# Kernel tuning notes

Hardware: AMD Instinct MI355X
Metric: run time of the kernel (lower is better)

Reference implementation:

```python
import jax, jax.numpy as jnp
import numpy as np

N_NODES = 100000


def setup_inputs() -> dict:
    key = jax.random.key(0)
    ks = jax.random.split(key, 7)
    n, d, c, e = N_NODES, 256, 128, 3200000
    features = jax.random.normal(ks[0], (n, d), dtype=jnp.float32)
    adj_row = jax.random.randint(ks[1], (e,), 0, n, dtype=jnp.int32)
    adj_col = jax.random.randint(ks[2], (e,), 0, n, dtype=jnp.int32)
    adj_vals = jax.random.uniform(ks[3], (e,), dtype=jnp.float32)
    kernel = jax.random.normal(ks[4], (d, c), dtype=jnp.float32) * (1.0 / np.sqrt(d))
    bias = jax.random.normal(ks[5], (c,), dtype=jnp.float32) * 0.01
    skip_weight = jax.random.normal(ks[6], (c,), dtype=jnp.float32)
    return {"features": features, "adj_row": adj_row, "adj_col": adj_col,
            "adj_vals": adj_vals, "kernel": kernel, "bias": bias,
            "skip_weight": skip_weight}


def reference(features, adj_row, adj_col, adj_vals, kernel, bias, skip_weight):
    # h = X @ W  : [n, c]
    h = features @ kernel
    # SpMM: out[r] += A[r, c] * h[c] over edges (COO)
    msgs = adj_vals[:, None] * h[adj_col]            # [e, c]
    agg = jax.ops.segment_sum(msgs, adj_row, num_segments=N_NODES)  # [n, c]
    out = h * skip_weight + agg                      # skip-connection scale + aggregation
    out = out + bias
    return jax.nn.selu(out)
```

## Files before the change

### kernel.cpp

```cpp
#include <hip/hip_runtime.h>
#include <math.h>

#define N_NODES 100000
#define D 256
#define C 128
#define N_EDGES 3200000

#define BROWS 64
#define NBUCKET ((N_NODES + BROWS - 1) / BROWS)
#define CAP 2432
#define EPB 8192
#define PBLOCKS ((N_EDGES + EPB - 1) / EPB)

#define GROWS 128
#define NGB ((N_NODES + GROWS - 1) / GROWS)
#define KH 128
#define XPAD 136

typedef __attribute__((ext_vector_type(8))) short bf16x8;
typedef __attribute__((ext_vector_type(4))) float f32x4;

__device__ __forceinline__ unsigned short f2bf(float f) {
  const unsigned int u = __float_as_uint(f);
  return (unsigned short)((u + 0x7fffu + ((u >> 16) & 1u)) >> 16);
}
__device__ __forceinline__ unsigned int pack_bf(float lo, float hi) {
  return (unsigned int)f2bf(lo) | ((unsigned int)f2bf(hi) << 16);
}
__device__ __forceinline__ float bflo(unsigned int u) {
  return __uint_as_float(u << 16);
}
__device__ __forceinline__ float bfhi(unsigned int u) {
  return __uint_as_float(u & 0xffff0000u);
}
__device__ __forceinline__ float selu1(float x) {
  const float scale = 1.0507009873554804934193349852946f;
  const float alpha = 1.6732632423543772848170429916717f;
  return x > 0.f ? scale * x : scale * alpha * (__expf(x) - 1.f);
}
__device__ __forceinline__ unsigned int pack_rec(int col, float val) {
  return ((unsigned int)col << 15) | ((unsigned int)f2bf(val) & 0x7fffu);
}
__device__ __forceinline__ float rec_val(unsigned int r) {
  return __uint_as_float((r & 0x7fffu) << 16);
}
__device__ __forceinline__ bf16x8 packA_nt(const float* p) {
  const f32x4 a0 = __builtin_nontemporal_load(reinterpret_cast<const f32x4*>(p));
  const f32x4 a1 =
      __builtin_nontemporal_load(reinterpret_cast<const f32x4*>(p) + 1);
  union {
    unsigned int u[4];
    bf16x8 v;
  } af;
  af.u[0] = pack_bf(a0[0], a0[1]);
  af.u[1] = pack_bf(a0[2], a0[3]);
  af.u[2] = pack_bf(a1[0], a1[1]);
  af.u[3] = pack_bf(a1[2], a1[3]);
  return af.v;
}

__global__ __launch_bounds__(256) void prep(const float* __restrict__ W,
                                            unsigned short* __restrict__ WT) {
  const int t = blockIdx.x * blockDim.x + threadIdx.x;
  const int n = t >> 8;
  const int k = t & 255;
  WT[t] = f2bf(W[k * C + n]);
}

__global__ __launch_bounds__(512) void gemm_partition(
    const float* __restrict__ X, const unsigned short* __restrict__ WT,
    unsigned short* __restrict__ h2, const int* __restrict__ row,
    const int* __restrict__ col, const float* __restrict__ vals,
    unsigned int* __restrict__ meta, uint2* __restrict__ recs) {
  __shared__ alignas(16) char smem[GROWS * XPAD * 2];
  const int bid = blockIdx.x;
  const int tid = threadIdx.x;
  const int rem = bid % 3;

  if (rem != 2) {
    unsigned short(*xs)[XPAD] = reinterpret_cast<unsigned short(*)[XPAD]>(smem);
    const int gid = (bid / 3) * 2 + rem;
    const int rows0 = gid * GROWS;
    const int lane = tid & 63;
    const int w = tid >> 6;
    const int r = lane & 15;
    const int kg = lane >> 4;

    f32x4 acc[8];
#pragma unroll
    for (int f = 0; f < 8; ++f) acc[f] = (f32x4){0.f, 0.f, 0.f, 0.f};

#pragma unroll
    for (int h = 0; h < 2; ++h) {
#pragma unroll
      for (int i = 0; i < 8; ++i) {
        const int lrow = w * 16 + i * 2 + (lane >> 5);
        const int grow = rows0 + lrow;
        const int kc = (lane & 31) * 4;
        f32x4 x = (f32x4){0.f, 0.f, 0.f, 0.f};
        if (grow < N_NODES)
          x = *reinterpret_cast<const f32x4*>(X + (size_t)grow * D + h * KH +
                                              kc);
        const unsigned int p0 = pack_bf(x[0], x[1]);
        const unsigned int p1 = pack_bf(x[2], x[3]);
        *reinterpret_cast<uint2*>(&xs[lrow][kc]) = make_uint2(p0, p1);
      }
      __syncthreads();
#pragma unroll
      for (int ks = 0; ks < 4; ++ks) {
        const bf16x8 a =
            *reinterpret_cast<const bf16x8*>(&xs[w * 16 + r][ks * 32 + kg * 8]);
#pragma unroll
        for (int f = 0; f < 8; ++f) {
          const bf16x8 bf = *reinterpret_cast<const bf16x8*>(
              WT + (size_t)(f * 16 + r) * D + h * KH + ks * 32 + kg * 8);
          acc[f] =
              __builtin_amdgcn_mfma_f32_16x16x32_bf16(a, bf, acc[f], 0, 0, 0);
        }
      }
      __syncthreads();
    }
#pragma unroll
    for (int f = 0; f < 8; ++f)
#pragma unroll
      for (int j = 0; j < 4; ++j) {
        const int grow = rows0 + w * 16 + kg * 4 + j;
        if (grow < N_NODES) h2[(size_t)grow * C + f * 16 + r] = f2bf(acc[f][j]);
      }
  } else {
    int* hist = reinterpret_cast<int*>(smem);
    int* scanA = reinterpret_cast<int*>(smem + 8192);
    int* scanB = reinterpret_cast<int*>(smem + 16384);
    const int pb = bid / 3;
    const int e0 = pb * EPB;
    for (int i = tid; i < NBUCKET; i += 512) hist[i] = 0;
    __syncthreads();

    unsigned int stash[16];
#pragma unroll
    for (int k = 0; k < 16; ++k) {
      const int e = e0 + k * 512 + tid;
      unsigned int s = 0xFFFFFFFFu;
      if (e < N_EDGES) {
        const int r = __builtin_nontemporal_load(row + e);
        const int off = atomicAdd(&hist[r >> 6], 1);
        s = (unsigned int)r | ((unsigned int)off << 17);
      }
      stash[k] = s;
    }
    __syncthreads();

    for (int i = tid; i < 2048; i += 512) scanA[i] = (i < NBUCKET) ? hist[i] : 0;
    __syncthreads();
    int* src = scanA;
    int* dst = scanB;
    for (int off = 1; off < 2048; off <<= 1) {
      for (int i = tid; i < 2048; i += 512)
        dst[i] = src[i] + ((i >= off) ? src[i - off] : 0);
      __syncthreads();
      int* tp = src;
      src = dst;
      dst = tp;
    }
    for (int b = tid; b < NBUCKET; b += 512) {
      const int sb = src[b] - hist[b];
      dst[b] = sb;
      meta[(size_t)pb * NBUCKET + b] =
          ((unsigned int)sb << 16) | (unsigned int)hist[b];
    }
    __syncthreads();

#pragma unroll
    for (int k = 0; k < 16; ++k) {
      const unsigned int s = stash[k];
      if (s == 0xFFFFFFFFu) continue;
      const int r = (int)(s & 0x1FFFFu);
      const int off = (int)(s >> 17);
      const int e = e0 + k * 512 + tid;
      const int c = __builtin_nontemporal_load(col + e);
      const float v = __builtin_nontemporal_load(vals + e);
      const int b = r >> 6;
      recs[(size_t)pb * EPB + dst[b] + off] =
          make_uint2(pack_rec(c, v), r & (BROWS - 1));
    }
  }
}

__global__ __launch_bounds__(256) void sort_gather_selu(
    const unsigned int* __restrict__ meta, const uint2* __restrict__ recs,
    const unsigned int* __restrict__ h2u, const float* __restrict__ skip,
    const float* __restrict__ bias, float* __restrict__ out) {
  __shared__ unsigned int sorted[CAP];
  __shared__ int hist[BROWS];
  __shared__ int start[BROWS];
  __shared__ int segA[512];
  __shared__ int segB[512];
  __shared__ unsigned int segglob[512];
  const int tid = threadIdx.x;
  const int b = blockIdx.x;

  for (int s = tid; s < 512; s += 256) {
    int cnt = 0;
    unsigned int gg = 0;
    if (s < PBLOCKS) {
      const unsigned int m = meta[(size_t)s * NBUCKET + b];
      cnt = (int)(m & 0xFFFFu);
      gg = (unsigned int)s * EPB + (m >> 16);
    }
    segA[s] = cnt;
    segglob[s] = gg;
  }
  if (tid < BROWS) hist[tid] = 0;
  __syncthreads();
  int* s1 = segA;
  int* s2 = segB;
  for (int off = 1; off < 512; off <<= 1) {
    for (int i = tid; i < 512; i += 256)
      s2[i] = s1[i] + ((i >= off) ? s1[i - off] : 0);
    __syncthreads();
    int* tp = s1;
    s1 = s2;
    s2 = tp;
  }
  const int fill0 = s1[PBLOCKS - 1];
  const int fill = fill0 < CAP ? fill0 : CAP;

  uint2 stash[10];
  int nst = 0;
  for (int i = tid; i < fill; i += 256) {
    int lo = 0, hi = PBLOCKS - 1;
    while (lo < hi) {
      const int mid = (lo + hi) >> 1;
      if (s1[mid] > i) hi = mid;
      else lo = mid + 1;
    }
    const int idx = i - (lo ? s1[lo - 1] : 0);
    const unsigned long long rc = __builtin_nontemporal_load(
        reinterpret_cast<const unsigned long long*>(recs) + segglob[lo] + idx);
    const unsigned int cv = (unsigned int)rc;
    const unsigned int lr = (unsigned int)(rc >> 32);
    const int off = atomicAdd(&hist[lr], 1);
    stash[nst] = make_uint2(cv, lr | ((unsigned int)off << 6));
    ++nst;
  }
  __syncthreads();

  if (tid < BROWS) start[tid] = hist[tid];
  __syncthreads();
  for (int off = 1; off < BROWS; off <<= 1) {
    int t = 0;
    if (tid < BROWS && tid >= off) t = start[tid - off];
    __syncthreads();
    if (tid < BROWS) start[tid] += t;
    __syncthreads();
  }

  for (int k = 0; k < nst; ++k) {
    const int lr = (int)(stash[k].y & 63u);
    const int off = (int)(stash[k].y >> 6);
    const int pos = start[lr] - hist[lr] + off;
    if (pos < CAP) sorted[pos] = stash[k].x;
  }
  __syncthreads();

  const int lane = tid & 63;
  const int wv = tid >> 6;
  for (int lr = wv; lr < BROWS; lr += 4) {
    const int grow = b * BROWS + lr;
    if (grow >= N_NODES) break;
    int j = start[lr] - hist[lr];
    int je = start[lr];
    if (je > CAP) je = CAP;
    if (j > je) j = je;
    float ax = 0.f, ay = 0.f;
    for (; j + 7 < je; j += 8) {
      unsigned int cc[8], uu[8];
#pragma unroll
      for (int q = 0; q < 8; ++q) cc[q] = sorted[j + q];
#pragma unroll
      for (int q = 0; q < 8; ++q) uu[q] = h2u[(size_t)(cc[q] >> 15) * 64 + lane];
#pragma unroll
      for (int q = 0; q < 8; ++q) {
        ax = fmaf(rec_val(cc[q]), bflo(uu[q]), ax);
        ay = fmaf(rec_val(cc[q]), bfhi(uu[q]), ay);
      }
    }
    for (; j + 3 < je; j += 4) {
      unsigned int cc[4], uu[4];
#pragma unroll
      for (int q = 0; q < 4; ++q) cc[q] = sorted[j + q];
#pragma unroll
      for (int q = 0; q < 4; ++q) uu[q] = h2u[(size_t)(cc[q] >> 15) * 64 + lane];
#pragma unroll
      for (int q = 0; q < 4; ++q) {
        ax = fmaf(rec_val(cc[q]), bflo(uu[q]), ax);
        ay = fmaf(rec_val(cc[q]), bfhi(uu[q]), ay);
      }
    }
    for (; j < je; ++j) {
      const unsigned int cc = sorted[j];
      const unsigned int u = h2u[(size_t)(cc >> 15) * 64 + lane];
      ax = fmaf(rec_val(cc), bflo(u), ax);
      ay = fmaf(rec_val(cc), bfhi(u), ay);
    }
    const unsigned int hr = h2u[(size_t)grow * 64 + lane];
    const float2 sk = *reinterpret_cast<const float2*>(skip + lane * 2);
    const float2 bi = *reinterpret_cast<const float2*>(bias + lane * 2);
    const float ox = selu1(fmaf(bflo(hr), sk.x, ax) + bi.x);
    const float oy = selu1(fmaf(bfhi(hr), sk.y, ay) + bi.y);
    *reinterpret_cast<float2*>(out + (size_t)grow * C + lane * 2) =
        make_float2(ox, oy);
  }
}

extern "C" void kernel_launch(void* const* d_in, const int* in_sizes, int n_in,
                              void* d_out, int out_size, void* d_ws,
                              size_t ws_size, hipStream_t stream) {
  const float* features = (const float*)d_in[0];
  const int* adj_row = (const int*)d_in[1];
  const int* adj_col = (const int*)d_in[2];
  const float* adj_vals = (const float*)d_in[3];
  const float* W = (const float*)d_in[4];
  const float* bias = (const float*)d_in[5];
  const float* skip = (const float*)d_in[6];
  float* out = (float*)d_out;

  char* ws = (char*)d_ws;
  const size_t SZ_H2 = (size_t)N_NODES * C * 2;
  const size_t OFF_RECS = (SZ_H2 + 255) & ~(size_t)255;
  const size_t SZ_RECS = (size_t)PBLOCKS * EPB * 8;
  const size_t OFF_META = OFF_RECS + SZ_RECS;
  const size_t SZ_META = (size_t)PBLOCKS * NBUCKET * 4;
  const size_t OFF_WT = (OFF_META + SZ_META + 255) & ~(size_t)255;
  const size_t NEEDED = OFF_WT + (size_t)D * C * 2;

  if (ws_size < NEEDED) return;

  unsigned short* h2 = (unsigned short*)ws;
  uint2* recs = (uint2*)(ws + OFF_RECS);
  unsigned int* meta = (unsigned int*)(ws + OFF_META);
  unsigned short* WT = (unsigned short*)(ws + OFF_WT);

  prep<<<(D * C) / 256, 256, 0, stream>>>(W, WT);

  gemm_partition<<<3 * PBLOCKS, 512, 0, stream>>>(
      features, WT, h2, adj_row, adj_col, adj_vals, meta, recs);

  sort_gather_selu<<<NBUCKET, 256, 0, stream>>>(
      meta, recs, (const unsigned int*)h2, skip, bias, out);
}
```

Baseline: 271.6 us.

## Co-schedule GEMM with bucket sort and split partition into its own kernel

Edge partitioning moves into a standalone kernel. The per-bucket sort now runs alongside the GEMM in one heterogeneous launch, writing sorted records and row pointers to global memory. A lean gather+SELU kernel then reads the presorted data. This aims to hide the sort under the GEMM and shorten the gather kernel, at the cost of an extra launch and an extra global round trip for the sorted records.

```diff
diff --git a/kernel.cpp b/kernel.cpp
--- a/kernel.cpp
+++ b/kernel.cpp
@@ -43,20 +43,6 @@
 }
 __device__ __forceinline__ float rec_val(unsigned int r) {
   return __uint_as_float((r & 0x7fffu) << 16);
-}
-__device__ __forceinline__ bf16x8 packA_nt(const float* p) {
-  const f32x4 a0 = __builtin_nontemporal_load(reinterpret_cast<const f32x4*>(p));
-  const f32x4 a1 =
-      __builtin_nontemporal_load(reinterpret_cast<const f32x4*>(p) + 1);
-  union {
-    unsigned int u[4];
-    bf16x8 v;
-  } af;
-  af.u[0] = pack_bf(a0[0], a0[1]);
-  af.u[1] = pack_bf(a0[2], a0[3]);
-  af.u[2] = pack_bf(a1[0], a1[1]);
-  af.u[3] = pack_bf(a1[2], a1[3]);
-  return af.v;
 }
 
 __global__ __launch_bounds__(256) void prep(const float* __restrict__ W,
@@ -67,19 +53,81 @@
   WT[t] = f2bf(W[k * C + n]);
 }
 
-__global__ __launch_bounds__(512) void gemm_partition(
+__global__ __launch_bounds__(512) void partition_kernel(
+    const int* __restrict__ row, const int* __restrict__ col,
+    const float* __restrict__ vals, unsigned int* __restrict__ meta,
+    uint2* __restrict__ recs) {
+  __shared__ int hist[2048];
+  __shared__ int scanA[2048];
+  __shared__ int scanB[2048];
+  const int pb = blockIdx.x;
+  const int tid = threadIdx.x;
+  const int e0 = pb * EPB;
+  for (int i = tid; i < NBUCKET; i += 512) hist[i] = 0;
+  __syncthreads();
+
+  unsigned int stash[16];
+#pragma unroll
+  for (int k = 0; k < 16; ++k) {
+    const int e = e0 + k * 512 + tid;
+    unsigned int s = 0xFFFFFFFFu;
+    if (e < N_EDGES) {
+      const int r = __builtin_nontemporal_load(row + e);
+      const int off = atomicAdd(&hist[r >> 6], 1);
+      s = (unsigned int)r | ((unsigned int)off << 17);
+    }
+    stash[k] = s;
+  }
+  __syncthreads();
+
+  for (int i = tid; i < 2048; i += 512) scanA[i] = (i < NBUCKET) ? hist[i] : 0;
+  __syncthreads();
+  int* src = scanA;
+  int* dst = scanB;
+  for (int off = 1; off < 2048; off <<= 1) {
+    for (int i = tid; i < 2048; i += 512)
+      dst[i] = src[i] + ((i >= off) ? src[i - off] : 0);
+    __syncthreads();
+    int* tp = src;
+    src = dst;
+    dst = tp;
+  }
+  for (int b = tid; b < NBUCKET; b += 512) {
+    const int sb = src[b] - hist[b];
+    dst[b] = sb;
+    meta[(size_t)pb * NBUCKET + b] =
+        ((unsigned int)sb << 16) | (unsigned int)hist[b];
+  }
+  __syncthreads();
+
+#pragma unroll
+  for (int k = 0; k < 16; ++k) {
+    const unsigned int s = stash[k];
+    if (s == 0xFFFFFFFFu) continue;
+    const int r = (int)(s & 0x1FFFFu);
+    const int off = (int)(s >> 17);
+    const int e = e0 + k * 512 + tid;
+    const int c = __builtin_nontemporal_load(col + e);
+    const float v = __builtin_nontemporal_load(vals + e);
+    const int b = r >> 6;
+    recs[(size_t)pb * EPB + dst[b] + off] =
+        make_uint2(pack_rec(c, v), r & (BROWS - 1));
+  }
+}
+
+__global__ __launch_bounds__(512) void gemm_sort(
     const float* __restrict__ X, const unsigned short* __restrict__ WT,
-    unsigned short* __restrict__ h2, const int* __restrict__ row,
-    const int* __restrict__ col, const float* __restrict__ vals,
-    unsigned int* __restrict__ meta, uint2* __restrict__ recs) {
+    unsigned short* __restrict__ h2, const unsigned int* __restrict__ meta,
+    const uint2* __restrict__ recs, unsigned int* __restrict__ sorted_g,
+    int* __restrict__ rowptr_g) {
   __shared__ alignas(16) char smem[GROWS * XPAD * 2];
   const int bid = blockIdx.x;
   const int tid = threadIdx.x;
   const int rem = bid % 3;
 
-  if (rem != 2) {
+  if (rem == 0) {
     unsigned short(*xs)[XPAD] = reinterpret_cast<unsigned short(*)[XPAD]>(smem);
-    const int gid = (bid / 3) * 2 + rem;
+    const int gid = bid / 3;
     const int rows0 = gid * GROWS;
     const int lane = tid & 63;
     const int w = tid >> 6;
@@ -128,155 +176,108 @@
         if (grow < N_NODES) h2[(size_t)grow * C + f * 16 + r] = f2bf(acc[f][j]);
       }
   } else {
-    int* hist = reinterpret_cast<int*>(smem);
-    int* scanA = reinterpret_cast<int*>(smem + 8192);
-    int* scanB = reinterpret_cast<int*>(smem + 16384);
-    const int pb = bid / 3;
-    const int e0 = pb * EPB;
-    for (int i = tid; i < NBUCKET; i += 512) hist[i] = 0;
-    __syncthreads();
-
-    unsigned int stash[16];
-#pragma unroll
-    for (int k = 0; k < 16; ++k) {
-      const int e = e0 + k * 512 + tid;
-      unsigned int s = 0xFFFFFFFFu;
-      if (e < N_EDGES) {
-        const int r = __builtin_nontemporal_load(row + e);
-        const int off = atomicAdd(&hist[r >> 6], 1);
-        s = (unsigned int)r | ((unsigned int)off << 17);
-      }
-      stash[k] = s;
-    }
-    __syncthreads();
-
-    for (int i = tid; i < 2048; i += 512) scanA[i] = (i < NBUCKET) ? hist[i] : 0;
-    __syncthreads();
-    int* src = scanA;
-    int* dst = scanB;
-    for (int off = 1; off < 2048; off <<= 1) {
-      for (int i = tid; i < 2048; i += 512)
-        dst[i] = src[i] + ((i >= off) ? src[i - off] : 0);
-      __syncthreads();
-      int* tp = src;
-      src = dst;
-      dst = tp;
-    }
-    for (int b = tid; b < NBUCKET; b += 512) {
-      const int sb = src[b] - hist[b];
-      dst[b] = sb;
-      meta[(size_t)pb * NBUCKET + b] =
-          ((unsigned int)sb << 16) | (unsigned int)hist[b];
-    }
-    __syncthreads();
-
-#pragma unroll
-    for (int k = 0; k < 16; ++k) {
-      const unsigned int s = stash[k];
-      if (s == 0xFFFFFFFFu) continue;
-      const int r = (int)(s & 0x1FFFFu);
-      const int off = (int)(s >> 17);
-      const int e = e0 + k * 512 + tid;
-      const int c = __builtin_nontemporal_load(col + e);
-      const float v = __builtin_nontemporal_load(vals + e);
-      const int b = r >> 6;
-      recs[(size_t)pb * EPB + dst[b] + off] =
-          make_uint2(pack_rec(c, v), r & (BROWS - 1));
-    }
-  }
-}
-
-__global__ __launch_bounds__(256) void sort_gather_selu(
-    const unsigned int* __restrict__ meta, const uint2* __restrict__ recs,
+    unsigned int* sorted = reinterpret_cast<unsigned int*>(smem);
+    int* segA = reinterpret_cast<int*>(smem + 9728);
+    int* segB = reinterpret_cast<int*>(smem + 9728 + 2048);
+    unsigned int* segglob =
+        reinterpret_cast<unsigned int*>(smem + 9728 + 4096);
+    int* hist = reinterpret_cast<int*>(smem + 9728 + 6144);
+    int* start = reinterpret_cast<int*>(smem + 9728 + 6400);
+
+    const int b = (bid / 3) * 2 + (rem - 1);
+
+    if (tid < PBLOCKS) {
+      const unsigned int m = meta[(size_t)tid * NBUCKET + b];
+      segA[tid] = (int)(m & 0xFFFFu);
+      segglob[tid] = (unsigned int)tid * EPB + (m >> 16);
+    } else {
+      segA[tid] = 0;
+      segglob[tid] = 0;
+    }
+    if (tid < BROWS) hist[tid] = 0;
+    __syncthreads();
+    int* s1 = segA;
+    int* s2 = segB;
+    for (int off = 1; off < 512; off <<= 1) {
+      s2[tid] = s1[tid] + ((tid >= off) ? s1[tid - off] : 0);
+      __syncthreads();
+      int* tp = s1;
+      s1 = s2;
+      s2 = tp;
+    }
+    const int fill0 = s1[PBLOCKS - 1];
+    const int fill = fill0 < CAP ? fill0 : CAP;
+
+    uint2 stash[5];
+    int nst = 0;
+    for (int i = tid; i < fill; i += 512) {
+      int lo = 0, hi = PBLOCKS - 1;
+      while (lo < hi) {
+        const int mid = (lo + hi) >> 1;
+        if (s1[mid] > i) hi = mid;
+        else lo = mid + 1;
+      }
+      const int idx = i - (lo ? s1[lo - 1] : 0);
+      const unsigned long long rc = __builtin_nontemporal_load(
+          reinterpret_cast<const unsigned long long*>(recs) + segglob[lo] +
+          idx);
+      const unsigned int cv = (unsigned int)rc;
+      const unsigned int lr = (unsigned int)(rc >> 32);
+      const int off = atomicAdd(&hist[lr], 1);
+      stash[nst] = make_uint2(cv, lr | ((unsigned int)off << 6));
+      ++nst;
+    }
+    __syncthreads();
+
+    if (tid < BROWS) start[tid] = hist[tid];
+    __syncthreads();
+    for (int off = 1; off < BROWS; off <<= 1) {
+      int t = 0;
+      if (tid < BROWS && tid >= off) t = start[tid - off];
+      __syncthreads();
+      if (tid < BROWS) start[tid] += t;
+      __syncthreads();
+    }
+
+    for (int k = 0; k < nst; ++k) {
+      const int lr = (int)(stash[k].y & 63u);
+      const int off = (int)(stash[k].y >> 6);
+      const int pos = start[lr] - hist[lr] + off;
+      if (pos < CAP) sorted[pos] = stash[k].x;
+    }
+    __syncthreads();
+
+    for (int i = tid; i < fill; i += 512)
+      sorted_g[(size_t)b * CAP + i] = sorted[i];
+    if (tid < BROWS) {
+      const int rp = start[tid];
+      rowptr_g[b * BROWS + tid] = rp < CAP ? rp : CAP;
+    }
+  }
+}
+
+__global__ __launch_bounds__(256) void gather_selu(
+    const unsigned int* __restrict__ sorted_g, const int* __restrict__ rowptr_g,
     const unsigned int* __restrict__ h2u, const float* __restrict__ skip,
     const float* __restrict__ bias, float* __restrict__ out) {
-  __shared__ unsigned int sorted[CAP];
-  __shared__ int hist[BROWS];
-  __shared__ int start[BROWS];
-  __shared__ int segA[512];
-  __shared__ int segB[512];
-  __shared__ unsigned int segglob[512];
   const int tid = threadIdx.x;
   const int b = blockIdx.x;
-
-  for (int s = tid; s < 512; s += 256) {
-    int cnt = 0;
-    unsigned int gg = 0;
-    if (s < PBLOCKS) {
-      const unsigned int m = meta[(size_t)s * NBUCKET + b];
-      cnt = (int)(m & 0xFFFFu);
-      gg = (unsigned int)s * EPB + (m >> 16);
-    }
-    segA[s] = cnt;
-    segglob[s] = gg;
-  }
-  if (tid < BROWS) hist[tid] = 0;
-  __syncthreads();
-  int* s1 = segA;
-  int* s2 = segB;
-  for (int off = 1; off < 512; off <<= 1) {
-    for (int i = tid; i < 512; i += 256)
-      s2[i] = s1[i] + ((i >= off) ? s1[i - off] : 0);
-    __syncthreads();
-    int* tp = s1;
-    s1 = s2;
-    s2 = tp;
-  }
-  const int fill0 = s1[PBLOCKS - 1];
-  const int fill = fill0 < CAP ? fill0 : CAP;
-
-  uint2 stash[10];
-  int nst = 0;
-  for (int i = tid; i < fill; i += 256) {
-    int lo = 0, hi = PBLOCKS - 1;
-    while (lo < hi) {
-      const int mid = (lo + hi) >> 1;
-      if (s1[mid] > i) hi = mid;
-      else lo = mid + 1;
-    }
-    const int idx = i - (lo ? s1[lo - 1] : 0);
-    const unsigned long long rc = __builtin_nontemporal_load(
-        reinterpret_cast<const unsigned long long*>(recs) + segglob[lo] + idx);
-    const unsigned int cv = (unsigned int)rc;
-    const unsigned int lr = (unsigned int)(rc >> 32);
-    const int off = atomicAdd(&hist[lr], 1);
-    stash[nst] = make_uint2(cv, lr | ((unsigned int)off << 6));
-    ++nst;
-  }
-  __syncthreads();
-
-  if (tid < BROWS) start[tid] = hist[tid];
-  __syncthreads();
-  for (int off = 1; off < BROWS; off <<= 1) {
-    int t = 0;
-    if (tid < BROWS && tid >= off) t = start[tid - off];
-    __syncthreads();
-    if (tid < BROWS) start[tid] += t;
-    __syncthreads();
-  }
-
-  for (int k = 0; k < nst; ++k) {
-    const int lr = (int)(stash[k].y & 63u);
-    const int off = (int)(stash[k].y >> 6);
-    const int pos = start[lr] - hist[lr] + off;
-    if (pos < CAP) sorted[pos] = stash[k].x;
-  }
-  __syncthreads();
-
   const int lane = tid & 63;
   const int wv = tid >> 6;
+  const int* rp = rowptr_g + b * BROWS;
+  const unsigned int* sg = sorted_g + (size_t)b * CAP;
+
   for (int lr = wv; lr < BROWS; lr += 4) {
     const int grow = b * BROWS + lr;
     if (grow >= N_NODES) break;
-    int j = start[lr] - hist[lr];
-    int je = start[lr];
-    if (je > CAP) je = CAP;
-    if (j > je) j = je;
+    int j = lr ? rp[lr - 1] : 0;
+    const int je = rp[lr];
     float ax = 0.f, ay = 0.f;
     for (; j + 7 < je; j += 8) {
       unsigned int cc[8], uu[8];
 #pragma unroll
-      for (int q = 0; q < 8; ++q) cc[q] = sorted[j + q];
+      for (int q = 0; q < 8; ++q)
+        cc[q] = __builtin_nontemporal_load(sg + j + q);
 #pragma unroll
       for (int q = 0; q < 8; ++q) uu[q] = h2u[(size_t)(cc[q] >> 15) * 64 + lane];
 #pragma unroll
@@ -288,7 +289,8 @@
     for (; j + 3 < je; j += 4) {
       unsigned int cc[4], uu[4];
 #pragma unroll
-      for (int q = 0; q < 4; ++q) cc[q] = sorted[j + q];
+      for (int q = 0; q < 4; ++q)
+        cc[q] = __builtin_nontemporal_load(sg + j + q);
 #pragma unroll
       for (int q = 0; q < 4; ++q) uu[q] = h2u[(size_t)(cc[q] >> 15) * 64 + lane];
 #pragma unroll
@@ -298,7 +300,7 @@
       }
     }
     for (; j < je; ++j) {
-      const unsigned int cc = sorted[j];
+      const unsigned int cc = __builtin_nontemporal_load(sg + j);
       const unsigned int u = h2u[(size_t)(cc >> 15) * 64 + lane];
       ax = fmaf(rec_val(cc), bflo(u), ax);
       ay = fmaf(rec_val(cc), bfhi(u), ay);
@@ -331,7 +333,11 @@
   const size_t SZ_RECS = (size_t)PBLOCKS * EPB * 8;
   const size_t OFF_META = OFF_RECS + SZ_RECS;
   const size_t SZ_META = (size_t)PBLOCKS * NBUCKET * 4;
-  const size_t OFF_WT = (OFF_META + SZ_META + 255) & ~(size_t)255;
+  const size_t OFF_SRT = (OFF_META + SZ_META + 255) & ~(size_t)255;
+  const size_t SZ_SRT = (size_t)NBUCKET * CAP * 4;
+  const size_t OFF_RP = OFF_SRT + SZ_SRT;
+  const size_t SZ_RP = (size_t)NBUCKET * BROWS * 4;
+  const size_t OFF_WT = (OFF_RP + SZ_RP + 255) & ~(size_t)255;
   const size_t NEEDED = OFF_WT + (size_t)D * C * 2;
 
   if (ws_size < NEEDED) return;
@@ -339,13 +345,19 @@
   unsigned short* h2 = (unsigned short*)ws;
   uint2* recs = (uint2*)(ws + OFF_RECS);
   unsigned int* meta = (unsigned int*)(ws + OFF_META);
+  unsigned int* sorted_g = (unsigned int*)(ws + OFF_SRT);
+  int* rowptr_g = (int*)(ws + OFF_RP);
   unsigned short* WT = (unsigned short*)(ws + OFF_WT);
 
   prep<<<(D * C) / 256, 256, 0, stream>>>(W, WT);
 
-  gemm_partition<<<3 * PBLOCKS, 512, 0, stream>>>(
-      features, WT, h2, adj_row, adj_col, adj_vals, meta, recs);
-
-  sort_gather_selu<<<NBUCKET, 256, 0, stream>>>(
-      meta, recs, (const unsigned int*)h2, skip, bias, out);
-}
+  partition_kernel<<<PBLOCKS, 512, 0, stream>>>(adj_row, adj_col, adj_vals,
+                                                meta, recs);
+
+  gemm_sort<<<NGB * 3 - 1, 512, 0, stream>>>(features, WT, h2, meta, recs,
+                                             sorted_g, rowptr_g);
+
+  gather_selu<<<NBUCKET, 256, 0, stream>>>(sorted_g, rowptr_g,
+                                           (const unsigned int*)h2, skip, bias,
+                                           out);
+}
```

Measured after the change: 314.9 us. +16.0%, slower.
